# Optimization experiments

Measured on AMD Instinct MI355X. Metric: run time of the kernel, lower is better.

The kernel has to match this reference:

```python
import jax, jax.numpy as jnp
import numpy as np

N = 50000      # nodes
E = 800000     # edges (before self-loops)
F_IN = 256     # num_features
NCLS = 8       # num_classes


def setup_inputs() -> dict:
    key = jax.random.key(0)
    ks = jax.random.split(key, 24)
    s = 0.05
    rn = lambda k, shape: jax.random.normal(k, shape, jnp.float32) * s
    return {
        "x": jax.random.normal(ks[0], (N, F_IN), jnp.float32),
        "edge_index": jax.random.randint(ks[1], (2, E), 0, N, dtype=jnp.int32),
        "w1": rn(ks[2], (F_IN, 512)), "b1": jnp.zeros((512,), jnp.float32),
        "w2": rn(ks[3], (512, 256)), "b2": jnp.zeros((256,), jnp.float32),
        "w3": rn(ks[4], (256, 128)), "b3": jnp.zeros((128,), jnp.float32),
        "wc1": rn(ks[5], (128, 256)), "as1": rn(ks[6], (4, 64)), "ad1": rn(ks[7], (4, 64)), "bc1": jnp.zeros((256,), jnp.float32),
        "wc2": rn(ks[8], (256, 128)), "as2": rn(ks[9], (4, 32)), "ad2": rn(ks[10], (4, 32)), "bc2": jnp.zeros((128,), jnp.float32),
        "wc3": rn(ks[11], (128, 8)), "as3": rn(ks[12], (1, 8)), "ad3": rn(ks[13], (1, 8)), "bc3": jnp.zeros((8,), jnp.float32),
    }


def _gat_conv(x, src, dst, W, att_src, att_dst, bias, heads, out_ch, concat):
    """PyG GATConv (eval mode): gather -> LeakyReLU attn -> segment softmax -> scatter-add."""
    n = x.shape[0]
    h = (x @ W).reshape(n, heads, out_ch)                  # [N,H,C]
    a_src = jnp.einsum('nhc,hc->nh', h, att_src)           # [N,H]
    a_dst = jnp.einsum('nhc,hc->nh', h, att_dst)           # [N,H]
    e = jax.nn.leaky_relu(a_src[src] + a_dst[dst], 0.2)    # [E,H]
    # numerically-stable softmax over edges grouped by destination node
    m = jax.ops.segment_max(e, dst, num_segments=n)        # [N,H]
    m = jnp.where(jnp.isfinite(m), m, 0.0)
    ex = jnp.exp(e - m[dst])
    denom = jax.ops.segment_sum(ex, dst, num_segments=n)   # [N,H]
    alpha = ex / jnp.maximum(denom[dst], 1e-16)            # [E,H]
    out = jax.ops.segment_sum(h[src] * alpha[:, :, None], dst, num_segments=n)  # [N,H,C]
    out = out.reshape(n, heads * out_ch) if concat else out.mean(axis=1)
    return out + bias


def reference(x, edge_index, w1, b1, w2, b2, w3, b3,
              wc1, as1, ad1, bc1, wc2, as2, ad2, bc2, wc3, as3, ad3, bc3):
    n = x.shape[0]
    # add self-loops (PyG GATConv default)
    loops = jnp.arange(n, dtype=edge_index.dtype)
    src = jnp.concatenate([edge_index[0], loops])
    dst = jnp.concatenate([edge_index[1], loops])

    h = jax.nn.relu(x @ w1 + b1)
    h = jax.nn.relu(h @ w2 + b2)
    h = jax.nn.relu(h @ w3 + b3)          # [N,128]; dropout inactive in eval

    h = jax.nn.elu(_gat_conv(h, src, dst, wc1, as1, ad1, bc1, 4, 64, True))   # [N,256]
    h = jax.nn.elu(_gat_conv(h, src, dst, wc2, as2, ad2, bc2, 4, 32, True))   # [N,128]
    out = _gat_conv(h, src, dst, wc3, as3, ad3, bc3, 1, NCLS, False)          # [N,8]
    return out
```

## Files before the change

### kernel.cpp

```cpp
#include <hip/hip_runtime.h>
#include <hip/hip_bf16.h>

#define NODES 50000
#define E0    800000
#define ETOT  (E0 + NODES)

typedef short  short8  __attribute__((ext_vector_type(8)));
typedef unsigned short ushort8 __attribute__((ext_vector_type(8)));
typedef float  f32x4   __attribute__((ext_vector_type(4)));
typedef __hip_bfloat16 bf16;

__device__ __forceinline__ float ldf(const float* p) { return *p; }
__device__ __forceinline__ float ldf(const bf16* p)  { return __bfloat162float(*p); }
__device__ __forceinline__ void  stf(float* p, float v) { *p = v; }
__device__ __forceinline__ void  stf(bf16* p, float v)  { *p = __float2bfloat16(v); }
__device__ __forceinline__ float bfbits(unsigned short u) {
    return __uint_as_float(((unsigned)u) << 16);
}
__device__ __forceinline__ float lrelu(float x) { return x > 0.f ? x : 0.2f * x; }
__device__ __forceinline__ float pick4(float4 v, int i) {
    float r = (i == 0) ? v.x : (i == 1) ? v.y : (i == 2) ? v.z : v.w;
    return r;
}

__device__ __forceinline__ void gload16(const void* g, unsigned short* l) {
    __builtin_amdgcn_global_load_lds(
        (const __attribute__((address_space(1))) unsigned int*)g,
        (__attribute__((address_space(3))) unsigned int*)l,
        16, 0, 0);
}

__global__ void f32_to_bf16(const float* __restrict__ in, bf16* __restrict__ out, int n4)
{
    int i = blockIdx.x * 256 + threadIdx.x;
    if (i >= n4) return;
    float4 v = *(const float4*)(in + (size_t)i * 4);
    bf16* o = out + (size_t)i * 4;
    o[0] = __float2bfloat16(v.x); o[1] = __float2bfloat16(v.y);
    o[2] = __float2bfloat16(v.z); o[3] = __float2bfloat16(v.w);
}

__global__ void w_transpose_bf16(const float* __restrict__ w, bf16* __restrict__ wt,
                                 int K, int N)
{
    int t = blockIdx.x * 256 + threadIdx.x;
    if (t >= K * N) return;
    int k = t / N, n = t % N;
    wt[(size_t)n * K + k] = __float2bfloat16(w[t]);
}

__global__ __launch_bounds__(256) void mfma_gemm(
    const bf16* __restrict__ A, const bf16* __restrict__ Bt,
    const float* __restrict__ bias, bf16* __restrict__ C,
    int M, int N, int K, int relu)
{
    __shared__ union {
        unsigned short AB[2][2][128 * 32];
        unsigned short Cs[128 * 136];
    } lds;

    const int tid  = threadIdx.x;
    const int wave = tid >> 6, lane = tid & 63;
    const int bm = blockIdx.y * 128, bn = blockIdx.x * 128;
    const int wr = (wave >> 1) * 64, wc = (wave & 1) * 64;
    const int lr = lane & 15, kg = lane >> 4;

    const int srow0 = tid >> 2, sko = (tid & 3) * 8;
    const int srow1 = srow0 + 64;
    int arow0 = bm + srow0; if (arow0 >= M) arow0 = M - 1;
    int arow1 = bm + srow1; if (arow1 >= M) arow1 = M - 1;
    const unsigned short* gA0 = (const unsigned short*)A + (size_t)arow0 * K + sko;
    const unsigned short* gA1 = (const unsigned short*)A + (size_t)arow1 * K + sko;
    const unsigned short* gB0 = (const unsigned short*)Bt + (size_t)(bn + srow0) * K + sko;
    const unsigned short* gB1 = (const unsigned short*)Bt + (size_t)(bn + srow1) * K + sko;

    f32x4 acc[4][4];
    #pragma unroll
    for (int m = 0; m < 4; m++)
        #pragma unroll
        for (int n = 0; n < 4; n++)
            #pragma unroll
            for (int j = 0; j < 4; j++) acc[m][n][j] = 0.f;

    const int nk = K >> 5;

    #define STAGE(buf, kk)                                              \
        gload16(gA0 + ((kk) << 5), &lds.AB[buf][0][tid * 8]);           \
        gload16(gA1 + ((kk) << 5), &lds.AB[buf][0][(tid + 256) * 8]);   \
        gload16(gB0 + ((kk) << 5), &lds.AB[buf][1][tid * 8]);           \
        gload16(gB1 + ((kk) << 5), &lds.AB[buf][1][(tid + 256) * 8]);

    STAGE(0, 0)
    __syncthreads();

    int cur = 0;
    for (int k = 0; k < nk; k++) {
        if (k + 1 < nk) {
            STAGE(cur ^ 1, k + 1)
        }
        short8 af[4], bfr[4];
        #pragma unroll
        for (int m = 0; m < 4; m++)
            af[m] = *(const short8*)&lds.AB[cur][0][(wr + m * 16 + lr) * 32 + kg * 8];
        #pragma unroll
        for (int n = 0; n < 4; n++)
            bfr[n] = *(const short8*)&lds.AB[cur][1][(wc + n * 16 + lr) * 32 + kg * 8];
        #pragma unroll
        for (int m = 0; m < 4; m++)
            #pragma unroll
            for (int n = 0; n < 4; n++)
                acc[m][n] = __builtin_amdgcn_mfma_f32_16x16x32_bf16(af[m], bfr[n], acc[m][n], 0, 0, 0);
        __syncthreads();
        cur ^= 1;
    }
    #undef STAGE

    #pragma unroll
    for (int m = 0; m < 4; m++) {
        #pragma unroll
        for (int n = 0; n < 4; n++) {
            const int col = wc + n * 16 + lr;
            const float bv = bias ? bias[bn + col] : 0.f;
            #pragma unroll
            for (int j = 0; j < 4; j++) {
                const int r = wr + m * 16 + kg * 4 + j;
                float v = acc[m][n][j] + bv;
                if (relu) v = fmaxf(v, 0.f);
                lds.Cs[r * 136 + col] = __bfloat16_as_ushort(__float2bfloat16(v));
            }
        }
    }
    __syncthreads();
    {
        const int row = tid >> 1, hf2 = tid & 1;
        const int gr = bm + row;
        if (gr < M) {
            const unsigned short* srcp = &lds.Cs[row * 136 + hf2 * 64];
            unsigned short* dstp = (unsigned short*)C + (size_t)gr * N + bn + hf2 * 64;
            #pragma unroll
            for (int i = 0; i < 8; i++)
                *(uint4*)(dstp + i * 8) = *(const uint4*)(srcp + i * 8);
        }
    }
}

__global__ void gemm_n8(const bf16* __restrict__ A, const float* __restrict__ B,
                        float* __restrict__ C, int M, int K)
{
    int t = blockIdx.x * 256 + threadIdx.x;
    int m = t >> 3, n = t & 7;
    if (m >= M) return;
    float s = 0.f;
    const ushort8* A8 = (const ushort8*)(A + (size_t)m * K);
    #pragma unroll 4
    for (int k8 = 0; k8 < K / 8; k8++) {
        ushort8 a = A8[k8];
        #pragma unroll
        for (int j = 0; j < 8; j++)
            s += bfbits(a[j]) * B[(k8 * 8 + j) * 8 + n];
    }
    C[t] = s;
}

template<int C>
__global__ void attn_scores_b(const bf16* __restrict__ hc, const float* __restrict__ att_s,
                              const float* __restrict__ att_d, float* __restrict__ aS,
                              float* __restrict__ aD, int npairs)
{
    constexpr int L = C / 8;
    int t = blockIdx.x * 256 + threadIdx.x;
    int gp = t / L, sub = t % L;
    if (gp >= npairs) return;
    int h = gp & 3;
    ushort8 v = *(const ushort8*)((const unsigned short*)hc + (size_t)gp * C + sub * 8);
    const float* as8 = att_s + h * C + sub * 8;
    const float* ad8 = att_d + h * C + sub * 8;
    float vs = 0.f, vd = 0.f;
    #pragma unroll
    for (int k = 0; k < 8; k++) {
        float f = bfbits(v[k]);
        vs += f * as8[k];
        vd += f * ad8[k];
    }
    #pragma unroll
    for (int off = L >> 1; off; off >>= 1) {
        vs += __shfl_xor(vs, off);
        vd += __shfl_xor(vd, off);
    }
    if (sub == 0) { aS[gp] = vs; aD[gp] = vd; }
}

__global__ void attn_scores_f(const float* __restrict__ hc, const float* __restrict__ att_s,
                              const float* __restrict__ att_d, float* __restrict__ aS,
                              float* __restrict__ aD, int nwaves)
{
    int gw = (blockIdx.x * blockDim.x + threadIdx.x) >> 6;
    int lane = threadIdx.x & 63;
    if (gw >= nwaves) return;
    float vs = 0.f, vd = 0.f;
    if (lane < 8) {
        float xv = hc[(size_t)gw * 8 + lane];
        vs = xv * att_s[lane];
        vd = xv * att_d[lane];
    }
    #pragma unroll
    for (int off = 4; off; off >>= 1) {
        vs += __shfl_xor(vs, off);
        vd += __shfl_xor(vd, off);
    }
    if (lane == 0) { aS[gw] = vs; aD[gw] = vd; }
}

__device__ __forceinline__ void edge_sd(int e, int& s, int& d,
                                        const int* __restrict__ src,
                                        const int* __restrict__ dst) {
    if (e < E0) { s = src[e]; d = dst[e]; } else { s = e - E0; d = s; }
}

__global__ void deg_hist(const int* __restrict__ src, const int* __restrict__ dst,
                         int* __restrict__ deg)
{
    int e = blockIdx.x * 256 + threadIdx.x;
    if (e >= ETOT) return;
    int s, d; edge_sd(e, s, d, src, dst);
    atomicAdd(&deg[d], 1);
}

__global__ void scan_block(const int* __restrict__ deg, int* __restrict__ ptr,
                           int* __restrict__ bsum, int n)
{
    __shared__ int sm[256];
    int t = threadIdx.x, i = blockIdx.x * 256 + t;
    int v = (i < n) ? deg[i] : 0;
    sm[t] = v; __syncthreads();
    #pragma unroll
    for (int off = 1; off < 256; off <<= 1) {
        int x = (t >= off) ? sm[t - off] : 0;
        __syncthreads();
        sm[t] += x; __syncthreads();
    }
    if (i < n) ptr[i] = sm[t] - v;
    if (t == 255) bsum[blockIdx.x] = sm[255];
}

__global__ void scan_bsum(int* __restrict__ bsum, int nb)
{
    __shared__ int sm[256];
    int t = threadIdx.x;
    int v = (t < nb) ? bsum[t] : 0;
    sm[t] = v; __syncthreads();
    #pragma unroll
    for (int off = 1; off < 256; off <<= 1) {
        int x = (t >= off) ? sm[t - off] : 0;
        __syncthreads();
        sm[t] += x; __syncthreads();
    }
    if (t < nb) bsum[t] = sm[t] - v;
}

__global__ void scan_add(int* __restrict__ ptr, const int* __restrict__ bsum, int n)
{
    int i = blockIdx.x * 256 + threadIdx.x;
    if (i < n) ptr[i] += bsum[blockIdx.x];
    if (i == 0) ptr[n] = ETOT;
}

__global__ void csr_fill(const int* __restrict__ src, const int* __restrict__ dst,
                         const int* __restrict__ ptr, int* __restrict__ cursor,
                         int* __restrict__ csr)
{
    int e = blockIdx.x * 256 + threadIdx.x;
    if (e >= ETOT) return;
    int s, d; edge_sd(e, s, d, src, dst);
    int pos = ptr[d] + atomicAdd(&cursor[d], 1);
    csr[pos] = s;
}

template<int C>
__global__ __launch_bounds__(256) void gat_wave(
    const bf16* __restrict__ hf, const float* __restrict__ aSv,
    const float* __restrict__ aDv, const int* __restrict__ ptr,
    const int* __restrict__ csr, const float* __restrict__ bias,
    bf16* __restrict__ out, int elu)
{
    constexpr int W   = 4 * C;
    constexpr int LPE = W / 8;
    constexpr int EPI = 64 / LPE;
    constexpr int CS  = (C == 64) ? 3 : 2;

    __shared__ int   ls[4][64];
    __shared__ float lwT[4][4][68];

    const int wv = threadIdx.x >> 6, lane = threadIdx.x & 63;
    const int d = blockIdx.x * 4 + wv;
    if (d >= NODES) return;
    const int beg = ptr[d], end = ptr[d + 1];

    const int lsub  = lane % LPE;
    const int h_own = lsub >> CS;
    const int ch0   = lsub * 8;

    const float4 aDd = *(const float4*)&aDv[d * 4];
    float4 den4 = {0.f, 0.f, 0.f, 0.f};
    float acc[8] = {};

    for (int tbeg = beg; tbeg < end; tbeg += 64) {
        const int nval = min(64, end - tbeg);

        if (lane < nval) {
            int s = csr[tbeg + lane];
            float4 a = *(const float4*)&aSv[s * 4];
            float4 ex;
            ex.x = __expf(lrelu(a.x + aDd.x));
            ex.y = __expf(lrelu(a.y + aDd.y));
            ex.z = __expf(lrelu(a.z + aDd.z));
            ex.w = __expf(lrelu(a.w + aDd.w));
            den4.x += ex.x; den4.y += ex.y; den4.z += ex.z; den4.w += ex.w;
            ls[wv][lane] = s;
            lwT[wv][0][lane] = ex.x;
            lwT[wv][1][lane] = ex.y;
            lwT[wv][2][lane] = ex.z;
            lwT[wv][3][lane] = ex.w;
        }

        for (int j = lane / LPE; j < nval; j += EPI) {
            const int   sj  = ls[wv][j];
            const float wgt = lwT[wv][h_own][j];
            ushort8 r = *(const ushort8*)((const unsigned short*)hf + (size_t)sj * W + ch0);
            #pragma unroll
            for (int k = 0; k < 8; k++) acc[k] += wgt * bfbits(r[k]);
        }
    }

    #pragma unroll
    for (int off = 32; off; off >>= 1) {
        den4.x += __shfl_xor(den4.x, off);
        den4.y += __shfl_xor(den4.y, off);
        den4.z += __shfl_xor(den4.z, off);
        den4.w += __shfl_xor(den4.w, off);
    }
    #pragma unroll
    for (int k = 0; k < 8; k++) {
        #pragma unroll
        for (int off = LPE; off < 64; off <<= 1)
            acc[k] += __shfl_xor(acc[k], off);
    }

    if (lane < LPE) {
        const float deno = fmaxf(pick4({den4.x, den4.y, den4.z, den4.w}, h_own), 1e-16f);
        const float rden = 1.f / deno;
        ushort8 o;
        #pragma unroll
        for (int k = 0; k < 8; k++) {
            float v = acc[k] * rden + bias[ch0 + k];
            if (elu) v = v > 0.f ? v : expm1f(v);
            o[k] = (unsigned short)(__bfloat16_as_ushort(__float2bfloat16(v)));
        }
        *(ushort8*)((unsigned short*)out + (size_t)d * W + ch0) = o;
    }
}

template<int H, int C, typename TIN, typename TOUT>
__global__ __launch_bounds__(256) void gat_fused(
    const TIN* __restrict__ hf, const float* __restrict__ aS,
    const float* __restrict__ aDv, const int* __restrict__ ptr,
    const int* __restrict__ csr, const float* __restrict__ bias,
    TOUT* __restrict__ out, int elu)
{
    constexpr int W = H * C;
    const int tl = threadIdx.x % W;
    const int dsub = threadIdx.x / W;
    const int d = blockIdx.x * (256 / W) + dsub;
    if (d >= NODES) return;
    const int h = tl / C, c = tl % C;
    const int beg = ptr[d], end = ptr[d + 1];
    const float aDd = aDv[d * H + h];

    float m = -1e30f, den = 0.f;
    for (int i = beg + c; i < end; i += C) {
        int s = csr[i];
        float e = aS[s * H + h] + aDd;
        e = e > 0.f ? e : 0.2f * e;
        float M = fmaxf(m, e);
        den = den * __expf(m - M) + __expf(e - M);
        m = M;
    }
    #pragma unroll
    for (int off = C >> 1; off; off >>= 1) {
        float mo = __shfl_xor(m, off);
        float dn = __shfl_xor(den, off);
        float M = fmaxf(m, mo);
        den = den * __expf(m - M) + dn * __expf(mo - M);
        m = M;
    }

    float acc = 0.f;
    for (int i = beg; i < end; i++) {
        int s = csr[i];
        float e = aS[s * H + h] + aDd;
        e = e > 0.f ? e : 0.2f * e;
        float w = __expf(e - m);
        acc += w * ldf(&hf[(size_t)s * W + tl]);
    }
    float v = acc / den + bias[tl];
    if (elu) v = v > 0.f ? v : expm1f(v);
    stf(&out[(size_t)d * W + tl], v);
}

extern "C" void kernel_launch(void* const* d_in, const int* in_sizes, int n_in,
                              void* d_out, int out_size, void* d_ws, size_t ws_size,
                              hipStream_t stream)
{
    const float* x   = (const float*)d_in[0];
    const int*   ei  = (const int*)d_in[1];
    const float* w1  = (const float*)d_in[2];  const float* b1  = (const float*)d_in[3];
    const float* w2  = (const float*)d_in[4];  const float* b2  = (const float*)d_in[5];
    const float* w3  = (const float*)d_in[6];  const float* b3  = (const float*)d_in[7];
    const float* wc1 = (const float*)d_in[8];  const float* as1 = (const float*)d_in[9];
    const float* ad1 = (const float*)d_in[10]; const float* bc1 = (const float*)d_in[11];
    const float* wc2 = (const float*)d_in[12]; const float* as2 = (const float*)d_in[13];
    const float* ad2 = (const float*)d_in[14]; const float* bc2 = (const float*)d_in[15];
    const float* wc3 = (const float*)d_in[16]; const float* as3 = (const float*)d_in[17];
    const float* ad3 = (const float*)d_in[18]; const float* bc3 = (const float*)d_in[19];

    const int* srcv = ei;
    const int* dstv = ei + E0;

    char* ws = (char*)d_ws;
    bf16*  xb    = (bf16*)(ws + 0);
    bf16*  h2b   = (bf16*)(ws + 0);
    bf16*  h1b   = (bf16*)(ws + 25600000);
    bf16*  hc1b  = (bf16*)(ws + 25600000);
    bf16*  out1b = (bf16*)(ws + 51200000);
    bf16*  h3b   = (bf16*)(ws + 76800000);
    bf16*  hc2b  = (bf16*)(ws + 76800000);
    bf16*  out2b = (bf16*)(ws + 89600000);
    float* hc3   = (float*)(ws + 102400000);
    float* aS    = (float*)(ws + 104000000);
    float* aD    = (float*)(ws + 104800000);
    int*   ptr   = (int*)  (ws + 105600000);
    int*   deg   = (int*)  (ws + 105900000);
    int*   bsum  = (int*)  (ws + 106200000);
    int*   csr   = (int*)  (ws + 106400000);
    bf16*  w1T   = (bf16*)(ws + 110000000);
    bf16*  w2T   = (bf16*)(ws + 110300000);
    bf16*  w3T   = (bf16*)(ws + 110600000);
    bf16*  wc1T  = (bf16*)(ws + 110700000);
    bf16*  wc2T  = (bf16*)(ws + 110800000);
    if (ws_size < (size_t)196000000) return;

    float* outf = (float*)d_out;
    dim3 blk(256);
    const int NB_SCAN = (NODES + 255) / 256;

    (void)hipMemsetAsync(deg, 0, (size_t)NODES * 4, stream);
    deg_hist<<<(ETOT + 255)/256, blk, 0, stream>>>(srcv, dstv, deg);
    scan_block<<<NB_SCAN, blk, 0, stream>>>(deg, ptr, bsum, NODES);
    scan_bsum<<<1, blk, 0, stream>>>(bsum, NB_SCAN);
    scan_add<<<NB_SCAN, blk, 0, stream>>>(ptr, bsum, NODES);
    (void)hipMemsetAsync(deg, 0, (size_t)NODES * 4, stream);
    csr_fill<<<(ETOT + 255)/256, blk, 0, stream>>>(srcv, dstv, ptr, deg, csr);

    f32_to_bf16<<<(NODES*256/4 + 255)/256, blk, 0, stream>>>(x, xb, NODES*256/4);
    w_transpose_bf16<<<(256*512 + 255)/256, blk, 0, stream>>>(w1, w1T, 256, 512);
    w_transpose_bf16<<<(512*256 + 255)/256, blk, 0, stream>>>(w2, w2T, 512, 256);
    w_transpose_bf16<<<(256*128 + 255)/256, blk, 0, stream>>>(w3, w3T, 256, 128);
    w_transpose_bf16<<<(128*256 + 255)/256, blk, 0, stream>>>(wc1, wc1T, 128, 256);
    w_transpose_bf16<<<(256*128 + 255)/256, blk, 0, stream>>>(wc2, wc2T, 256, 128);

    const int gy = (NODES + 127) / 128;
    mfma_gemm<<<dim3(4, gy), blk, 0, stream>>>(xb,  w1T, b1, h1b, NODES, 512, 256, 1);
    mfma_gemm<<<dim3(2, gy), blk, 0, stream>>>(h1b, w2T, b2, h2b, NODES, 256, 512, 1);
    mfma_gemm<<<dim3(1, gy), blk, 0, stream>>>(h2b, w3T, b3, h3b, NODES, 128, 256, 1);

    mfma_gemm<<<dim3(2, gy), blk, 0, stream>>>(h3b, wc1T, nullptr, hc1b, NODES, 256, 128, 0);
    attn_scores_b<64><<<(NODES*4*8 + 255)/256, blk, 0, stream>>>(hc1b, as1, ad1, aS, aD,
                                                                 NODES*4);
    gat_wave<64><<<(NODES + 3)/4, blk, 0, stream>>>(hc1b, aS, aD, ptr, csr, bc1, out1b, 1);

    mfma_gemm<<<dim3(1, gy), blk, 0, stream>>>(out1b, wc2T, nullptr, hc2b, NODES, 128, 256, 0);
    attn_scores_b<32><<<(NODES*4*4 + 255)/256, blk, 0, stream>>>(hc2b, as2, ad2, aS, aD,
                                                                 NODES*4);
    gat_wave<32><<<(NODES + 3)/4, blk, 0, stream>>>(hc2b, aS, aD, ptr, csr, bc2, out2b, 1);

    gemm_n8<<<(NODES*8 + 255)/256, blk, 0, stream>>>(out2b, wc3, hc3, NODES, 128);
    attn_scores_f<<<(NODES*64 + 255)/256, blk, 0, stream>>>(hc3, as3, ad3, aS, aD, NODES);
    gat_fused<1,8,float,float><<<(NODES + 31)/32, blk, 0, stream>>>(hc3, aS, aD, ptr, csr, bc3, outf, 0);
}
```

Baseline: 435.2 us.

## Fuse attention scores into GEMM epilogues and simplify the final GAT layer

Attention source and destination scores are now computed in the MFMA GEMM epilogue from the bf16 tile already staged in LDS, and in the 8-column GEMM through a shuffle reduction. This removes the separate attention-score kernels and a re-read of the projected features. The five weight-transpose launches are merged into one. The second memset is folded into the first by placing the CSR cursor array next to the degree array. The last GAT layer becomes a single pass with no running-max subtraction, which saves a traversal of the edge list but gives up the numerical protection that max subtraction provides against overflow in exp.

```diff
diff --git a/kernel.cpp b/kernel.cpp
--- a/kernel.cpp
+++ b/kernel.cpp
@@ -10,10 +10,6 @@
 typedef float  f32x4   __attribute__((ext_vector_type(4)));
 typedef __hip_bfloat16 bf16;
 
-__device__ __forceinline__ float ldf(const float* p) { return *p; }
-__device__ __forceinline__ float ldf(const bf16* p)  { return __bfloat162float(*p); }
-__device__ __forceinline__ void  stf(float* p, float v) { *p = v; }
-__device__ __forceinline__ void  stf(bf16* p, float v)  { *p = __float2bfloat16(v); }
 __device__ __forceinline__ float bfbits(unsigned short u) {
     return __uint_as_float(((unsigned)u) << 16);
 }
@@ -40,19 +36,32 @@
     o[2] = __float2bfloat16(v.z); o[3] = __float2bfloat16(v.w);
 }
 
-__global__ void w_transpose_bf16(const float* __restrict__ w, bf16* __restrict__ wt,
-                                 int K, int N)
-{
-    int t = blockIdx.x * 256 + threadIdx.x;
-    if (t >= K * N) return;
+__device__ __forceinline__ void wtr(const float* w, bf16* wt, int K, int N, int t)
+{
     int k = t / N, n = t % N;
     wt[(size_t)n * K + k] = __float2bfloat16(w[t]);
 }
 
+__global__ void w_transpose_all(
+    const float* w1, const float* w2, const float* w3,
+    const float* wc1, const float* wc2,
+    bf16* w1T, bf16* w2T, bf16* w3T, bf16* wc1T, bf16* wc2T)
+{
+    int t = blockIdx.x * 256 + threadIdx.x;
+    if      (t < 131072)  wtr(w1,  w1T,  256, 512, t);
+    else if (t < 262144)  wtr(w2,  w2T,  512, 256, t - 131072);
+    else if (t < 294912)  wtr(w3,  w3T,  256, 128, t - 262144);
+    else if (t < 327680)  wtr(wc1, wc1T, 128, 256, t - 294912);
+    else if (t < 360448)  wtr(wc2, wc2T, 256, 128, t - 327680);
+}
+
+template<int SLC>
 __global__ __launch_bounds__(256) void mfma_gemm(
     const bf16* __restrict__ A, const bf16* __restrict__ Bt,
     const float* __restrict__ bias, bf16* __restrict__ C,
-    int M, int N, int K, int relu)
+    int M, int N, int K, int relu,
+    const float* __restrict__ att_s, const float* __restrict__ att_d,
+    float* __restrict__ aSo, float* __restrict__ aDo)
 {
     __shared__ union {
         unsigned short AB[2][2][128 * 32];
@@ -137,21 +146,45 @@
         if (gr < M) {
             const unsigned short* srcp = &lds.Cs[row * 136 + hf2 * 64];
             unsigned short* dstp = (unsigned short*)C + (size_t)gr * N + bn + hf2 * 64;
-            #pragma unroll
-            for (int i = 0; i < 8; i++)
-                *(uint4*)(dstp + i * 8) = *(const uint4*)(srcp + i * 8);
-        }
-    }
-}
-
-__global__ void gemm_n8(const bf16* __restrict__ A, const float* __restrict__ B,
-                        float* __restrict__ C, int M, int K)
+            ushort8 chunk[8];
+            #pragma unroll
+            for (int i = 0; i < 8; i++) chunk[i] = *(const ushort8*)(srcp + i * 8);
+            #pragma unroll
+            for (int i = 0; i < 8; i++) *(ushort8*)(dstp + i * 8) = chunk[i];
+            if constexpr (SLC > 0) {
+                constexpr int NH = 64 / SLC;
+                const int seg0 = bn + hf2 * 64;
+                #pragma unroll
+                for (int hh = 0; hh < NH; hh++) {
+                    const int head = (seg0 >> (SLC == 64 ? 6 : 5)) + hh;
+                    const float* asv = att_s + head * SLC;
+                    const float* adv = att_d + head * SLC;
+                    float vs = 0.f, vd = 0.f;
+                    #pragma unroll
+                    for (int i = 0; i < SLC; i++) {
+                        const int idx = hh * SLC + i;
+                        float f = bfbits(chunk[idx >> 3][idx & 7]);
+                        vs = fmaf(f, asv[i], vs);
+                        vd = fmaf(f, adv[i], vd);
+                    }
+                    aSo[gr * 4 + head] = vs;
+                    aDo[gr * 4 + head] = vd;
+                }
+            }
+        }
+    }
+}
+
+__global__ void gemm_n8_scores(const bf16* __restrict__ A, const float* __restrict__ B,
+                               float* __restrict__ C, int M, int K,
+                               const float* __restrict__ as3, const float* __restrict__ ad3,
+                               float* __restrict__ aS, float* __restrict__ aD)
 {
     int t = blockIdx.x * 256 + threadIdx.x;
     int m = t >> 3, n = t & 7;
     if (m >= M) return;
     float s = 0.f;
-    const ushort8* A8 = (const ushort8*)(A + (size_t)m * K);
+    const ushort8* A8 = (const ushort8*)((const unsigned short*)A + (size_t)m * K);
     #pragma unroll 4
     for (int k8 = 0; k8 < K / 8; k8++) {
         ushort8 a = A8[k8];
@@ -160,55 +193,13 @@
             s += bfbits(a[j]) * B[(k8 * 8 + j) * 8 + n];
     }
     C[t] = s;
-}
-
-template<int C>
-__global__ void attn_scores_b(const bf16* __restrict__ hc, const float* __restrict__ att_s,
-                              const float* __restrict__ att_d, float* __restrict__ aS,
-                              float* __restrict__ aD, int npairs)
-{
-    constexpr int L = C / 8;
-    int t = blockIdx.x * 256 + threadIdx.x;
-    int gp = t / L, sub = t % L;
-    if (gp >= npairs) return;
-    int h = gp & 3;
-    ushort8 v = *(const ushort8*)((const unsigned short*)hc + (size_t)gp * C + sub * 8);
-    const float* as8 = att_s + h * C + sub * 8;
-    const float* ad8 = att_d + h * C + sub * 8;
-    float vs = 0.f, vd = 0.f;
-    #pragma unroll
-    for (int k = 0; k < 8; k++) {
-        float f = bfbits(v[k]);
-        vs += f * as8[k];
-        vd += f * ad8[k];
-    }
-    #pragma unroll
-    for (int off = L >> 1; off; off >>= 1) {
+    float vs = s * as3[n], vd = s * ad3[n];
+    #pragma unroll
+    for (int off = 1; off < 8; off <<= 1) {
         vs += __shfl_xor(vs, off);
         vd += __shfl_xor(vd, off);
     }
-    if (sub == 0) { aS[gp] = vs; aD[gp] = vd; }
-}
-
-__global__ void attn_scores_f(const float* __restrict__ hc, const float* __restrict__ att_s,
-                              const float* __restrict__ att_d, float* __restrict__ aS,
-                              float* __restrict__ aD, int nwaves)
-{
-    int gw = (blockIdx.x * blockDim.x + threadIdx.x) >> 6;
-    int lane = threadIdx.x & 63;
-    if (gw >= nwaves) return;
-    float vs = 0.f, vd = 0.f;
-    if (lane < 8) {
-        float xv = hc[(size_t)gw * 8 + lane];
-        vs = xv * att_s[lane];
-        vd = xv * att_d[lane];
-    }
-    #pragma unroll
-    for (int off = 4; off; off >>= 1) {
-        vs += __shfl_xor(vs, off);
-        vd += __shfl_xor(vd, off);
-    }
-    if (lane == 0) { aS[gw] = vs; aD[gw] = vd; }
+    if (n == 0) { aS[m] = vs; aD[m] = vd; }
 }
 
 __device__ __forceinline__ void edge_sd(int e, int& s, int& d,
@@ -360,51 +351,24 @@
     }
 }
 
-template<int H, int C, typename TIN, typename TOUT>
-__global__ __launch_bounds__(256) void gat_fused(
-    const TIN* __restrict__ hf, const float* __restrict__ aS,
-    const float* __restrict__ aDv, const int* __restrict__ ptr,
-    const int* __restrict__ csr, const float* __restrict__ bias,
-    TOUT* __restrict__ out, int elu)
-{
-    constexpr int W = H * C;
-    const int tl = threadIdx.x % W;
-    const int dsub = threadIdx.x / W;
-    const int d = blockIdx.x * (256 / W) + dsub;
+__global__ void gat3_onepass(const float* __restrict__ hc3, const float* __restrict__ aS,
+                             const float* __restrict__ aD, const int* __restrict__ ptr,
+                             const int* __restrict__ csr, const float* __restrict__ bias,
+                             float* __restrict__ out)
+{
+    int t = blockIdx.x * 256 + threadIdx.x;
+    int d = t >> 3, c = t & 7;
     if (d >= NODES) return;
-    const int h = tl / C, c = tl % C;
     const int beg = ptr[d], end = ptr[d + 1];
-    const float aDd = aDv[d * H + h];
-
-    float m = -1e30f, den = 0.f;
-    for (int i = beg + c; i < end; i += C) {
-        int s = csr[i];
-        float e = aS[s * H + h] + aDd;
-        e = e > 0.f ? e : 0.2f * e;
-        float M = fmaxf(m, e);
-        den = den * __expf(m - M) + __expf(e - M);
-        m = M;
-    }
-    #pragma unroll
-    for (int off = C >> 1; off; off >>= 1) {
-        float mo = __shfl_xor(m, off);
-        float dn = __shfl_xor(den, off);
-        float M = fmaxf(m, mo);
-        den = den * __expf(m - M) + dn * __expf(mo - M);
-        m = M;
-    }
-
-    float acc = 0.f;
+    const float aDd = aD[d];
+    float acc = 0.f, den = 0.f;
     for (int i = beg; i < end; i++) {
         int s = csr[i];
-        float e = aS[s * H + h] + aDd;
-        e = e > 0.f ? e : 0.2f * e;
-        float w = __expf(e - m);
-        acc += w * ldf(&hf[(size_t)s * W + tl]);
-    }
-    float v = acc / den + bias[tl];
-    if (elu) v = v > 0.f ? v : expm1f(v);
-    stf(&out[(size_t)d * W + tl], v);
+        float ex = __expf(lrelu(aS[s] + aDd));
+        den += ex;
+        acc += ex * hc3[s * 8 + c];
+    }
+    out[d * 8 + c] = acc / fmaxf(den, 1e-16f) + bias[c];
 }
 
 extern "C" void kernel_launch(void* const* d_in, const int* in_sizes, int n_in,
@@ -440,7 +404,8 @@
     float* aD    = (float*)(ws + 104800000);
     int*   ptr   = (int*)  (ws + 105600000);
     int*   deg   = (int*)  (ws + 105900000);
-    int*   bsum  = (int*)  (ws + 106200000);
+    int*   curs  = (int*)  (ws + 106100000);
+    int*   bsum  = (int*)  (ws + 106300000);
     int*   csr   = (int*)  (ws + 106400000);
     bf16*  w1T   = (bf16*)(ws + 110000000);
     bf16*  w2T   = (bf16*)(ws + 110300000);
@@ -453,37 +418,34 @@
     dim3 blk(256);
     const int NB_SCAN = (NODES + 255) / 256;
 
-    (void)hipMemsetAsync(deg, 0, (size_t)NODES * 4, stream);
+    (void)hipMemsetAsync(deg, 0, (size_t)400000, stream);
     deg_hist<<<(ETOT + 255)/256, blk, 0, stream>>>(srcv, dstv, deg);
     scan_block<<<NB_SCAN, blk, 0, stream>>>(deg, ptr, bsum, NODES);
     scan_bsum<<<1, blk, 0, stream>>>(bsum, NB_SCAN);
     scan_add<<<NB_SCAN, blk, 0, stream>>>(ptr, bsum, NODES);
-    (void)hipMemsetAsync(deg, 0, (size_t)NODES * 4, stream);
-    csr_fill<<<(ETOT + 255)/256, blk, 0, stream>>>(srcv, dstv, ptr, deg, csr);
+    csr_fill<<<(ETOT + 255)/256, blk, 0, stream>>>(srcv, dstv, ptr, curs, csr);
 
     f32_to_bf16<<<(NODES*256/4 + 255)/256, blk, 0, stream>>>(x, xb, NODES*256/4);
-    w_transpose_bf16<<<(256*512 + 255)/256, blk, 0, stream>>>(w1, w1T, 256, 512);
-    w_transpose_bf16<<<(512*256 + 255)/256, blk, 0, stream>>>(w2, w2T, 512, 256);
-    w_transpose_bf16<<<(256*128 + 255)/256, blk, 0, stream>>>(w3, w3T, 256, 128);
-    w_transpose_bf16<<<(128*256 + 255)/256, blk, 0, stream>>>(wc1, wc1T, 128, 256);
-    w_transpose_bf16<<<(256*128 + 255)/256, blk, 0, stream>>>(wc2, wc2T, 256, 128);
+    w_transpose_all<<<(360448 + 255)/256, blk, 0, stream>>>(w1, w2, w3, wc1, wc2,
+                                                            w1T, w2T, w3T, wc1T, wc2T);
 
     const int gy = (NODES + 127) / 128;
-    mfma_gemm<<<dim3(4, gy), blk, 0, stream>>>(xb,  w1T, b1, h1b, NODES, 512, 256, 1);
-    mfma_gemm<<<dim3(2, gy), blk, 0, stream>>>(h1b, w2T, b2, h2b, NODES, 256, 512, 1);
-    mfma_gemm<<<dim3(1, gy), blk, 0, stream>>>(h2b, w3T, b3, h3b, NODES, 128, 256, 1);
-
-    mfma_gemm<<<dim3(2, gy), blk, 0, stream>>>(h3b, wc1T, nullptr, hc1b, NODES, 256, 128, 0);
-    attn_scores_b<64><<<(NODES*4*8 + 255)/256, blk, 0, stream>>>(hc1b, as1, ad1, aS, aD,
-                                                                 NODES*4);
+    mfma_gemm<0><<<dim3(4, gy), blk, 0, stream>>>(xb,  w1T, b1, h1b, NODES, 512, 256, 1,
+                                                  nullptr, nullptr, nullptr, nullptr);
+    mfma_gemm<0><<<dim3(2, gy), blk, 0, stream>>>(h1b, w2T, b2, h2b, NODES, 256, 512, 1,
+                                                  nullptr, nullptr, nullptr, nullptr);
+    mfma_gemm<0><<<dim3(1, gy), blk, 0, stream>>>(h2b, w3T, b3, h3b, NODES, 128, 256, 1,
+                                                  nullptr, nullptr, nullptr, nullptr);
+
+    mfma_gemm<64><<<dim3(2, gy), blk, 0, stream>>>(h3b, wc1T, nullptr, hc1b, NODES, 256, 128, 0,
+                                                   as1, ad1, aS, aD);
     gat_wave<64><<<(NODES + 3)/4, blk, 0, stream>>>(hc1b, aS, aD, ptr, csr, bc1, out1b, 1);
 
-    mfma_gemm<<<dim3(1, gy), blk, 0, stream>>>(out1b, wc2T, nullptr, hc2b, NODES, 128, 256, 0);
-    attn_scores_b<32><<<(NODES*4*4 + 255)/256, blk, 0, stream>>>(hc2b, as2, ad2, aS, aD,
-                                                                 NODES*4);
+    mfma_gemm<32><<<dim3(1, gy), blk, 0, stream>>>(out1b, wc2T, nullptr, hc2b, NODES, 128, 256, 0,
+                                                   as2, ad2, aS, aD);
     gat_wave<32><<<(NODES + 3)/4, blk, 0, stream>>>(hc2b, aS, aD, ptr, csr, bc2, out2b, 1);
 
-    gemm_n8<<<(NODES*8 + 255)/256, blk, 0, stream>>>(out2b, wc3, hc3, NODES, 128);
-    attn_scores_f<<<(NODES*64 + 255)/256, blk, 0, stream>>>(hc3, as3, ad3, aS, aD, NODES);
-    gat_fused<1,8,float,float><<<(NODES + 31)/32, blk, 0, stream>>>(hc3, aS, aD, ptr, csr, bc3, outf, 0);
-}
+    gemm_n8_scores<<<(NODES*8 + 255)/256, blk, 0, stream>>>(out2b, wc3, hc3, NODES, 128,
+                                                            as3, ad3, aS, aD);
+    gat3_onepass<<<(NODES*8 + 255)/256, blk, 0, stream>>>(hc3, aS, aD, ptr, csr, bc3, outf);
+}
```

After: 420.5 us. 3.4% less time.
